# Performance work log

Measured on AMD Instinct MI355X. Metric: run time of the kernel, lower is better.

## Reference

```python
import jax, jax.numpy as jnp
import numpy as np
import math

N = 100000          # total nodes across all subgraphs
E = 1600000         # directed edges (avg degree 16)
H = 128             # hidden_channels
MAXZ = 1000         # max_z
G = 1000            # number of subgraphs (unique batch ids)
NPG = N // G        # nodes per subgraph
L = 3               # num_layers


def setup_inputs() -> dict:
    key = jax.random.key(0)
    ks = jax.random.split(key, 9)
    z = jax.random.randint(ks[0], (N,), 0, MAXZ, dtype=jnp.int32)
    edge_index = jax.random.randint(ks[1], (2, E), 0, N, dtype=jnp.int32)
    batch = jnp.repeat(jnp.arange(G, dtype=jnp.int32), NPG)  # sorted graph ids
    s = 1.0 / math.sqrt(H)
    z_emb_table = jax.random.normal(ks[2], (MAXZ, H), jnp.float32) * 0.1
    conv_w = jax.random.normal(ks[3], (L, H, H), jnp.float32) * s
    conv_b = jnp.zeros((L, H), jnp.float32)
    mlp_w1 = jax.random.normal(ks[4], (H, H), jnp.float32) * s
    mlp_b1 = jnp.zeros((H,), jnp.float32)
    mlp_w2 = jax.random.normal(ks[5], (H, 1), jnp.float32) * s
    mlp_b2 = jnp.zeros((1,), jnp.float32)
    return {"num_nodes": N, "z": z, "edge_index": edge_index, "batch": batch,
            "z_emb_table": z_emb_table, "conv_w": conv_w, "conv_b": conv_b,
            "mlp_w1": mlp_w1, "mlp_b1": mlp_b1, "mlp_w2": mlp_w2, "mlp_b2": mlp_b2}


def reference(num_nodes, z, edge_index, batch, z_emb_table, conv_w, conv_b,
              mlp_w1, mlp_b1, mlp_w2, mlp_b2):
    # --- GCN normalization (PyG GCNConv: add self-loops, sym deg norm) ---
    loops = jnp.arange(num_nodes, dtype=edge_index.dtype)
    src = jnp.concatenate([edge_index[0], loops])  # [E+N]
    dst = jnp.concatenate([edge_index[1], loops])
    deg = jax.ops.segment_sum(jnp.ones_like(dst, jnp.float32), dst,
                              num_segments=num_nodes)
    dinv = jnp.where(deg > 0, jax.lax.rsqrt(deg), 0.0)
    norm = (dinv[src] * dinv[dst])[:, None]        # [E+N, 1]

    # --- embedding lookup (eval mode: no dropedge/dropout) ---
    x = z_emb_table[z]                             # [N, H]

    # --- stacked GCNConv: linear -> gather -> normalize -> scatter-add ---
    for l in range(L):
        h = x @ conv_w[l]                          # [N, H]
        h = jax.ops.segment_sum(h[src] * norm, dst, num_segments=num_nodes)
        h = h + conv_b[l]
        x = jax.nn.relu(h) if l < L - 1 else h

    # --- center-node pooling: first occurrence of each batch id ---
    first = jnp.concatenate([jnp.array([True]), batch[1:] != batch[:-1]])
    ci = jnp.nonzero(first, size=G)[0]             # [G]
    xs = x[ci] * x[ci + 1]                         # src * dst node features

    # --- MLP head [H, H, 1] (batch_norm=False, eval: dropout off) ---
    h = jax.nn.relu(xs @ mlp_w1 + mlp_b1)
    return h @ mlp_w2 + mlp_b2                     # [G, 1]
```

## Files before the change

### kernel.cpp

```cpp
#include <hip/hip_runtime.h>
#include <hip/hip_fp16.h>

#define HD 128
#define BSH 9
#define NBLKA 256
#define CAP 96
#define EDSCAP 10240
#define CAPB 12288
#define XSW(row, c8) (((size_t)(row) << 7) + ((size_t)(((c8) ^ ((row) & 7))) << 3))

typedef _Float16 half8_t __attribute__((ext_vector_type(8)));
typedef float floatx4 __attribute__((ext_vector_type(4)));

__device__ inline unsigned pack_h2(float x, float y) {
  __half2 h = __floats2half2_rn(x, y);
  return __builtin_bit_cast(unsigned, h);
}
__device__ inline float2 up_h2(unsigned u) {
  __half2 h = __builtin_bit_cast(__half2, u);
  return __half22float2(h);
}

__device__ inline void add8(float* acc, uint4 r) {
  float2 f;
  f = up_h2(r.x); acc[0] += f.x; acc[1] += f.y;
  f = up_h2(r.y); acc[2] += f.x; acc[3] += f.y;
  f = up_h2(r.z); acc[4] += f.x; acc[5] += f.y;
  f = up_h2(r.w); acc[6] += f.x; acc[7] += f.y;
}

__global__ __launch_bounds__(256) void k_phase0(const int* __restrict__ src,
                                                const int* __restrict__ dst, int E, int nbuck,
                                                unsigned* __restrict__ bpool,
                                                int* __restrict__ counts,
                                                const float* __restrict__ conv_w,
                                                uint4* __restrict__ wfrag,
                                                const int* __restrict__ batch,
                                                int* __restrict__ ci,
                                                int* __restrict__ flag,
                                                int n) {
  __shared__ int cnt[512];
  int b = blockIdx.x;
  if (b < NBLKA) {
    for (int i = threadIdx.x; i < nbuck; i += 256) cnt[i] = 0;
    __syncthreads();
    int chunk = (E + NBLKA - 1) / NBLKA;
    int lo = b * chunk, hi = min(E, lo + chunk);
    for (int i = lo + threadIdx.x; i < hi; i += 256) {
      int s = src[i], d = dst[i];
      int bk = d >> BSH;
      int c = atomicAdd(&cnt[bk], 1);
      if (c < CAP)
        bpool[((size_t)bk * NBLKA + b) * CAP + c] =
            ((unsigned)(d & ((1 << BSH) - 1)) << 23) | (unsigned)s;
    }
    __syncthreads();
    for (int bk = threadIdx.x; bk < nbuck; bk += 256) counts[(size_t)bk * NBLKA + b] = cnt[bk];
  } else if (b < NBLKA + 24) {
    int t = (b - NBLKA) * 256 + threadIdx.x;
    int lane = t & 63;
    int s = (t >> 6) & 3;
    int c4 = (t >> 8) & 3;
    int chalf = (t >> 10) & 1;
    int layer = t >> 11;
    int col = chalf * 64 + c4 * 16 + (lane & 15);
    int k0 = s * 32 + (lane >> 4) * 8;
    const float* W = conv_w + (size_t)layer * HD * HD;
    unsigned u[4];
#pragma unroll
    for (int j = 0; j < 4; ++j)
      u[j] = pack_h2(W[(size_t)(k0 + 2 * j) * HD + col], W[(size_t)(k0 + 2 * j + 1) * HD + col]);
    uint4 o; o.x = u[0]; o.y = u[1]; o.z = u[2]; o.w = u[3];
    wfrag[t] = o;
  } else {
    int i = (b - NBLKA - 24) * 256 + threadIdx.x;
    if (i >= n) return;
    flag[i] = 0;
    if (i == 0) flag[n] = 0;
    if (i == 0 || batch[i] != batch[i - 1]) ci[batch[i]] = i;
  }
}

__global__ __launch_bounds__(256) void k_build(const unsigned* __restrict__ bpool,
                                               const int* __restrict__ counts,
                                               int n, float* __restrict__ dinv,
                                               int* __restrict__ rowstart,
                                               int* __restrict__ rowend,
                                               int* __restrict__ col) {
  __shared__ unsigned eds[EDSCAP];
  __shared__ int hist[1 << BSH];
  __shared__ int wsum[256];
  __shared__ int coff[NBLKA + 1];
  int b = blockIdx.x;
  int t = threadIdx.x;
  int v = (t < NBLKA) ? min(counts[(size_t)b * NBLKA + t], CAP) : 0;
  wsum[t] = v;
  __syncthreads();
  for (int off = 1; off < NBLKA; off <<= 1) {
    int x = (t >= off) ? wsum[t - off] : 0;
    __syncthreads();
    wsum[t] += x;
    __syncthreads();
  }
  if (t < NBLKA) coff[t] = wsum[t] - v;
  if (t == NBLKA - 1) coff[NBLKA] = wsum[NBLKA - 1];
  __syncthreads();
  int total = min(coff[NBLKA], EDSCAP);
  int w = t >> 6, lane = t & 63;
  for (int blk = w; blk < NBLKA; blk += 4) {
    int off0 = coff[blk], len = coff[blk + 1] - off0;
    const unsigned* seg = bpool + ((size_t)b * NBLKA + blk) * CAP;
    for (int i = lane; i < len; i += 64)
      if (off0 + i < EDSCAP) eds[off0 + i] = seg[i];
  }
  for (int i = t; i < (1 << BSH); i += 256) hist[i] = 0;
  __syncthreads();
  for (int i = t; i < total; i += 256) atomicAdd(&hist[eds[i] >> 23], 1);
  __syncthreads();
  int base = b << BSH;
  int nn = min(1 << BSH, n - base);
  int a0 = hist[2 * t], a1 = hist[2 * t + 1];
  int s = a0 + a1;
  wsum[t] = s;
  __syncthreads();
  for (int off = 1; off < 256; off <<= 1) {
    int x = (t >= off) ? wsum[t - off] : 0;
    __syncthreads();
    wsum[t] += x;
    __syncthreads();
  }
  int excl = wsum[t] - s;
  int cbase = b * CAPB;
  if (2 * t < nn) {
    rowstart[base + 2 * t] = cbase + excl;
    rowend[base + 2 * t] = cbase + excl + a0;
    dinv[base + 2 * t] = 1.0f / sqrtf((float)(a0 + 1));
  }
  if (2 * t + 1 < nn) {
    rowstart[base + 2 * t + 1] = cbase + excl + a0;
    rowend[base + 2 * t + 1] = cbase + excl + s;
    dinv[base + 2 * t + 1] = 1.0f / sqrtf((float)(a1 + 1));
  }
  hist[2 * t] = cbase + excl;
  hist[2 * t + 1] = cbase + excl + a0;
  __syncthreads();
  for (int i = t; i < total; i += 256) {
    unsigned pk = eds[i];
    int dl = pk >> 23;
    int pos = atomicAdd(&hist[dl], 1);
    col[pos] = (int)(pk & 0x7FFFFF);
  }
}

__global__ __launch_bounds__(64) void k_active(const int* __restrict__ ci,
                                               const int* __restrict__ rowstart,
                                               const int* __restrict__ rowend,
                                               const int* __restrict__ col,
                                               int g2, int* __restrict__ flag,
                                               int* __restrict__ list, int n) {
  int lane = threadIdx.x;
  int vid = blockIdx.x * 64 + lane;
  bool haveRow = vid < g2;
  int* nactive = flag + n;
  int node = 0, e = 0, end = 0;
  if (haveRow) {
    node = ci[vid >> 1] + (vid & 1);
    e = rowstart[node];
    end = rowend[node];
  }
  bool neu = haveRow && (atomicExch(&flag[node], 1) == 0);
  unsigned long long m = __ballot(neu);
  int base = 0;
  if (lane == 0 && m) base = atomicAdd(nactive, __popcll(m));
  base = __shfl(base, 0);
  if (neu) list[base + __popcll(m & ((1ULL << lane) - 1))] = node;
  for (;;) {
    bool act = haveRow && (e < end);
    if (!__any(act)) break;
    int s = act ? col[e] : 0;
    bool nw = act && (atomicExch(&flag[s], 1) == 0);
    unsigned long long mm = __ballot(nw);
    int b2 = 0;
    if (lane == 0 && mm) b2 = atomicAdd(nactive, __popcll(mm));
    b2 = __shfl(b2, 0);
    if (nw) list[b2 + __popcll(mm & ((1ULL << lane) - 1))] = s;
    ++e;
  }
}

__device__ inline void gemm16(const _Float16* xs, const uint4* __restrict__ wfragL,
                              const float* __restrict__ dinv, uint2* __restrict__ Yh,
                              int row0, int nvalid, const int* __restrict__ rowmap,
                              int tid) {
  int lane = tid & 63, w = tid >> 6;
  int chalf = w >> 1, h = lane >> 4;
  half8_t wf[8];
#pragma unroll
  for (int cc = 0; cc < 2; ++cc)
#pragma unroll
    for (int s = 0; s < 4; ++s) {
      int c4 = 2 * (w & 1) + cc;
      wf[cc * 4 + s] = __builtin_bit_cast(half8_t,
          wfragL[((chalf * 4 + c4) * 4 + s) * 64 + lane]);
    }
  half8_t bf[4];
#pragma unroll
  for (int s = 0; s < 4; ++s)
    bf[s] = *(const half8_t*)&xs[XSW(lane & 15, s * 4 + h)];
  floatx4 acc[2];
  acc[0] = (floatx4){0.f, 0.f, 0.f, 0.f};
  acc[1] = (floatx4){0.f, 0.f, 0.f, 0.f};
#pragma unroll
  for (int s = 0; s < 4; ++s) {
    acc[0] = __builtin_amdgcn_mfma_f32_16x16x32_f16(wf[s], bf[s], acc[0], 0, 0, 0);
    acc[1] = __builtin_amdgcn_mfma_f32_16x16x32_f16(wf[4 + s], bf[s], acc[1], 0, 0, 0);
  }
  int i = row0 + (lane & 15);
  if (i < nvalid) {
    int orow = rowmap ? rowmap[i] : i;
    float dv = dinv[orow];
#pragma unroll
    for (int cc = 0; cc < 2; ++cc) {
      int c4 = 2 * (w & 1) + cc;
      int colbase = chalf * 64 + c4 * 16 + h * 4;
      uint2 o;
      o.x = pack_h2(acc[cc][0] * dv, acc[cc][1] * dv);
      o.y = pack_h2(acc[cc][2] * dv, acc[cc][3] * dv);
      Yh[(size_t)orow * 32 + (colbase >> 2)] = o;
    }
  }
}

__global__ __launch_bounds__(256) void k_embgemm(const int* __restrict__ z,
                                                 const float4* __restrict__ emb,
                                                 const uint4* __restrict__ wfragL,
                                                 const float* __restrict__ dinv,
                                                 uint2* __restrict__ Yh, int n) {
  __shared__ __align__(16) _Float16 xs[16 * HD];
  int tid = threadIdx.x;
  int grp = tid >> 4, li = tid & 15;
  int node = blockIdx.x * 16 + grp;
  int nd = node < n ? node : n - 1;
  const float4* er = emb + (size_t)z[nd] * 32 + li * 2;
  float4 f0 = er[0], f1 = er[1];
  uint4 hx;
  hx.x = pack_h2(f0.x, f0.y); hx.y = pack_h2(f0.z, f0.w);
  hx.z = pack_h2(f1.x, f1.y); hx.w = pack_h2(f1.z, f1.w);
  *(uint4*)&xs[XSW(grp, li)] = hx;
  __syncthreads();
  gemm16(xs, wfragL, dinv, Yh, blockIdx.x * 16, n, nullptr, tid);
}

__global__ __launch_bounds__(256) void k_agg_gemm(const uint4* __restrict__ H,
                                                  const int* __restrict__ rowstart,
                                                  const int* __restrict__ rowend,
                                                  const int* __restrict__ col,
                                                  const float* __restrict__ dinv,
                                                  const float* __restrict__ bias,
                                                  const uint4* __restrict__ wfragL,
                                                  uint2* __restrict__ Yh, int n) {
  __shared__ __align__(16) _Float16 xs[16 * HD];
  int tid = threadIdx.x;
  int grp = tid >> 4, li = tid & 15;
  int node = blockIdx.x * 16 + grp;
  int nd = node < n ? node : n - 1;
  uint4 srow = H[(size_t)nd * 16 + li];
  float acc[8] = {0.f, 0.f, 0.f, 0.f, 0.f, 0.f, 0.f, 0.f};
  add8(acc, srow);
  int e = rowstart[nd], end = rowend[nd];
  for (; e + 3 < end; e += 4) {
    int c0 = col[e], c1 = col[e + 1], c2 = col[e + 2], c3 = col[e + 3];
    uint4 r0 = H[(size_t)c0 * 16 + li];
    uint4 r1 = H[(size_t)c1 * 16 + li];
    uint4 r2 = H[(size_t)c2 * 16 + li];
    uint4 r3 = H[(size_t)c3 * 16 + li];
    add8(acc, r0);
    add8(acc, r1);
    add8(acc, r2);
    add8(acc, r3);
  }
  for (; e < end; ++e) {
    uint4 r = H[(size_t)col[e] * 16 + li];
    add8(acc, r);
  }
  float dv = dinv[nd];
  float4 b0 = ((const float4*)bias)[2 * li];
  float4 b1 = ((const float4*)bias)[2 * li + 1];
  acc[0] = fmaxf(fmaf(dv, acc[0], b0.x), 0.f);
  acc[1] = fmaxf(fmaf(dv, acc[1], b0.y), 0.f);
  acc[2] = fmaxf(fmaf(dv, acc[2], b0.z), 0.f);
  acc[3] = fmaxf(fmaf(dv, acc[3], b0.w), 0.f);
  acc[4] = fmaxf(fmaf(dv, acc[4], b1.x), 0.f);
  acc[5] = fmaxf(fmaf(dv, acc[5], b1.y), 0.f);
  acc[6] = fmaxf(fmaf(dv, acc[6], b1.z), 0.f);
  acc[7] = fmaxf(fmaf(dv, acc[7], b1.w), 0.f);
  uint4 hx;
  hx.x = pack_h2(acc[0], acc[1]); hx.y = pack_h2(acc[2], acc[3]);
  hx.z = pack_h2(acc[4], acc[5]); hx.w = pack_h2(acc[6], acc[7]);
  *(uint4*)&xs[XSW(grp, li)] = hx;
  __syncthreads();
  gemm16(xs, wfragL, dinv, Yh, blockIdx.x * 16, n, nullptr, tid);
}

__global__ __launch_bounds__(256) void k_agg_gemmL(const uint4* __restrict__ H,
                                                   const int* __restrict__ rowstart,
                                                   const int* __restrict__ rowend,
                                                   const int* __restrict__ col,
                                                   const float* __restrict__ dinv,
                                                   const float* __restrict__ bias,
                                                   const uint4* __restrict__ wfragL,
                                                   uint2* __restrict__ Yh,
                                                   const int* __restrict__ list,
                                                   const int* __restrict__ nactive) {
  __shared__ __align__(16) _Float16 xs[16 * HD];
  int na = *nactive;
  int tid = threadIdx.x;
  int grp = tid >> 4, li = tid & 15;
  for (int tile = blockIdx.x; tile * 16 < na; tile += gridDim.x) {
    int i = tile * 16 + grp;
    int node = list[i < na ? i : na - 1];
    uint4 srow = H[(size_t)node * 16 + li];
    float acc[8] = {0.f, 0.f, 0.f, 0.f, 0.f, 0.f, 0.f, 0.f};
    add8(acc, srow);
    int e = rowstart[node], end = rowend[node];
    for (; e + 3 < end; e += 4) {
      int c0 = col[e], c1 = col[e + 1], c2 = col[e + 2], c3 = col[e + 3];
      uint4 r0 = H[(size_t)c0 * 16 + li];
      uint4 r1 = H[(size_t)c1 * 16 + li];
      uint4 r2 = H[(size_t)c2 * 16 + li];
      uint4 r3 = H[(size_t)c3 * 16 + li];
      add8(acc, r0);
      add8(acc, r1);
      add8(acc, r2);
      add8(acc, r3);
    }
    for (; e < end; ++e) {
      uint4 r = H[(size_t)col[e] * 16 + li];
      add8(acc, r);
    }
    float dv = dinv[node];
    float4 b0 = ((const float4*)bias)[2 * li];
    float4 b1 = ((const float4*)bias)[2 * li + 1];
    acc[0] = fmaxf(fmaf(dv, acc[0], b0.x), 0.f);
    acc[1] = fmaxf(fmaf(dv, acc[1], b0.y), 0.f);
    acc[2] = fmaxf(fmaf(dv, acc[2], b0.z), 0.f);
    acc[3] = fmaxf(fmaf(dv, acc[3], b0.w), 0.f);
    acc[4] = fmaxf(fmaf(dv, acc[4], b1.x), 0.f);
    acc[5] = fmaxf(fmaf(dv, acc[5], b1.y), 0.f);
    acc[6] = fmaxf(fmaf(dv, acc[6], b1.z), 0.f);
    acc[7] = fmaxf(fmaf(dv, acc[7], b1.w), 0.f);
    uint4 hx;
    hx.x = pack_h2(acc[0], acc[1]); hx.y = pack_h2(acc[2], acc[3]);
    hx.z = pack_h2(acc[4], acc[5]); hx.w = pack_h2(acc[6], acc[7]);
    *(uint4*)&xs[XSW(grp, li)] = hx;
    __syncthreads();
    gemm16(xs, wfragL, dinv, Yh, tile * 16, na, list, tid);
    __syncthreads();
  }
}

__global__ __launch_bounds__(128) void k_tail(const uint4* __restrict__ H,
                                              const int* __restrict__ rowstart,
                                              const int* __restrict__ rowend,
                                              const int* __restrict__ col,
                                              const float* __restrict__ dinv,
                                              const float* __restrict__ bias,
                                              const int* __restrict__ ci,
                                              const float* __restrict__ W1,
                                              const float* __restrict__ b1,
                                              const float* __restrict__ w2,
                                              const float* __restrict__ b2,
                                              float* __restrict__ out, int G) {
  __shared__ float part[8][HD];
  __shared__ float xs[HD];
  __shared__ float red[HD];
  int g = blockIdx.x;
  int t = threadIdx.x;
  int grp = t >> 4, li = t & 15;
  int nodeA = ci[g];
  int node = nodeA + (grp >> 2);
  int gi = grp & 3;
  float acc[8] = {0.f, 0.f, 0.f, 0.f, 0.f, 0.f, 0.f, 0.f};
  if (gi == 0) add8(acc, H[(size_t)node * 16 + li]);
  for (int e = rowstart[node] + gi; e < rowend[node]; e += 4) {
    uint4 r = H[(size_t)col[e] * 16 + li];
    add8(acc, r);
  }
#pragma unroll
  for (int j = 0; j < 8; ++j) part[grp][li * 8 + j] = acc[j];
  __syncthreads();
  float sumA = part[0][t] + part[1][t] + part[2][t] + part[3][t];
  float sumB = part[4][t] + part[5][t] + part[6][t] + part[7][t];
  float bb = bias[t];
  float va = fmaf(dinv[nodeA], sumA, bb);
  float vb = fmaf(dinv[nodeA + 1], sumB, bb);
  xs[t] = va * vb;
  __syncthreads();
  float hacc = b1[t];
#pragma unroll 8
  for (int k = 0; k < HD; ++k) hacc = fmaf(xs[k], W1[k * HD + t], hacc);
  hacc = fmaxf(hacc, 0.f);
  red[t] = hacc * w2[t];
  __syncthreads();
  for (int off = 64; off > 0; off >>= 1) {
    if (t < off) red[t] += red[t + off];
    __syncthreads();
  }
  if (t == 0) out[g] = red[0] + b2[0];
}

extern "C" void kernel_launch(void* const* d_in, const int* in_sizes, int n_in,
                              void* d_out, int out_size, void* d_ws, size_t ws_size,
                              hipStream_t stream) {
  (void)n_in; (void)ws_size;
  const int*   z      = (const int*)d_in[1];
  const int*   ei     = (const int*)d_in[2];
  const int*   batch  = (const int*)d_in[3];
  const float* emb    = (const float*)d_in[4];
  const float* conv_w = (const float*)d_in[5];
  const float* conv_b = (const float*)d_in[6];
  const float* w1     = (const float*)d_in[7];
  const float* b1     = (const float*)d_in[8];
  const float* w2     = (const float*)d_in[9];
  const float* b2     = (const float*)d_in[10];
  int n = in_sizes[1];
  int E = in_sizes[2] / 2;
  int G = out_size;
  const int* esrc = ei;
  const int* edst = ei + E;
  int nbuck = (n + (1 << BSH) - 1) >> BSH;

  char* p = (char*)d_ws;
  auto alloc = [&](size_t bytes) { void* r = (void*)p; p += (bytes + 255) / 256 * 256; return r; };
  unsigned* bufA     = (unsigned*)alloc((size_t)n * HD * 2);
  unsigned* bufB     = (unsigned*)alloc((size_t)n * HD * 2);
  float*    dinv     = (float*)alloc((size_t)n * 4);
  int*      rowstart = (int*)alloc((size_t)n * 4);
  int*      rowend   = (int*)alloc((size_t)n * 4);
  int*      col      = (int*)alloc((size_t)nbuck * CAPB * 4);
  uint4*    wfrag    = (uint4*)alloc((size_t)3 * 2048 * 16);
  int*      ci       = (int*)alloc((size_t)G * 4);
  int*      flag     = (int*)alloc((size_t)(n + 64) * 4);
  int*      list     = (int*)alloc((size_t)n * 4);
  unsigned* bpool    = (unsigned*)alloc((size_t)nbuck * NBLKA * CAP * 4);
  int*      counts   = (int*)alloc((size_t)nbuck * NBLKA * 4);

  int ciBlocks = (n + 255) / 256;
  int g2 = 2 * G;
  int* nactive = flag + n;

  k_phase0<<<NBLKA + 24 + ciBlocks, 256, 0, stream>>>(
      esrc, edst, E, nbuck, bpool, counts, conv_w, wfrag, batch, ci, flag, n);
  k_build<<<nbuck, 256, 0, stream>>>(bpool, counts, n, dinv, rowstart, rowend, col);
  k_embgemm<<<(n + 15) / 16, 256, 0, stream>>>(z, (const float4*)emb, wfrag, dinv,
                                               (uint2*)bufB, n);
  k_active<<<(g2 + 63) / 64, 64, 0, stream>>>(ci, rowstart, rowend, col, g2, flag, list, n);
  k_agg_gemm<<<(n + 15) / 16, 256, 0, stream>>>((const uint4*)bufB, rowstart, rowend, col,
                                                dinv, conv_b, wfrag + 2048, (uint2*)bufA, n);
  k_agg_gemmL<<<512, 256, 0, stream>>>((const uint4*)bufA, rowstart, rowend, col, dinv,
                                       conv_b + HD, wfrag + 4096, (uint2*)bufB, list, nactive);
  k_tail<<<G, 128, 0, stream>>>((const uint4*)bufB, rowstart, rowend, col, dinv,
                                conv_b + 2 * HD, ci, w1, b1, w2, b2, (float*)d_out, G);
}
```

Baseline: 226.8 us.

## Precompute embedding-times-weight table per z and gather it in first aggregation

Layer 0's linear transform is applied to the 1000-row embedding table instead of to every node, producing a small table T0 inside extra blocks of k_build. The first aggregation then gathers T0 rows indexed by z, with a packed (z, dinv) array per node, and scales each by the source dinv. This removes the per-node embedding GEMM kernel and the full-size fp16 intermediate write and read. It adds an extra indirection per edge, the D2 load, before the row gather.

New measurement: 200.1 us. -11.8%, faster.

```diff
diff --git a/kernel.cpp b/kernel.cpp
--- a/kernel.cpp
+++ b/kernel.cpp
@@ -27,6 +27,14 @@
   f = up_h2(r.y); acc[2] += f.x; acc[3] += f.y;
   f = up_h2(r.z); acc[4] += f.x; acc[5] += f.y;
   f = up_h2(r.w); acc[6] += f.x; acc[7] += f.y;
+}
+
+__device__ inline void fma8w(float* acc, uint4 r, float w) {
+  float2 f;
+  f = up_h2(r.x); acc[0] = fmaf(w, f.x, acc[0]); acc[1] = fmaf(w, f.y, acc[1]);
+  f = up_h2(r.y); acc[2] = fmaf(w, f.x, acc[2]); acc[3] = fmaf(w, f.y, acc[3]);
+  f = up_h2(r.z); acc[4] = fmaf(w, f.x, acc[4]); acc[5] = fmaf(w, f.y, acc[5]);
+  f = up_h2(r.w); acc[6] = fmaf(w, f.x, acc[6]); acc[7] = fmaf(w, f.y, acc[7]);
 }
 
 __global__ __launch_bounds__(256) void k_phase0(const int* __restrict__ src,
@@ -81,18 +89,83 @@
   }
 }
 
+__device__ inline void gemm16(const _Float16* xs, const uint4* __restrict__ wfragL,
+                              const float* __restrict__ dinv, uint2* __restrict__ Yh,
+                              int row0, int nvalid, const int* __restrict__ rowmap,
+                              int tid) {
+  int lane = tid & 63, w = tid >> 6;
+  int chalf = w >> 1, h = lane >> 4;
+  half8_t wf[8];
+#pragma unroll
+  for (int cc = 0; cc < 2; ++cc)
+#pragma unroll
+    for (int s = 0; s < 4; ++s) {
+      int c4 = 2 * (w & 1) + cc;
+      wf[cc * 4 + s] = __builtin_bit_cast(half8_t,
+          wfragL[((chalf * 4 + c4) * 4 + s) * 64 + lane]);
+    }
+  half8_t bf[4];
+#pragma unroll
+  for (int s = 0; s < 4; ++s)
+    bf[s] = *(const half8_t*)&xs[XSW(lane & 15, s * 4 + h)];
+  floatx4 acc[2];
+  acc[0] = (floatx4){0.f, 0.f, 0.f, 0.f};
+  acc[1] = (floatx4){0.f, 0.f, 0.f, 0.f};
+#pragma unroll
+  for (int s = 0; s < 4; ++s) {
+    acc[0] = __builtin_amdgcn_mfma_f32_16x16x32_f16(wf[s], bf[s], acc[0], 0, 0, 0);
+    acc[1] = __builtin_amdgcn_mfma_f32_16x16x32_f16(wf[4 + s], bf[s], acc[1], 0, 0, 0);
+  }
+  int i = row0 + (lane & 15);
+  if (i < nvalid) {
+    int orow = rowmap ? rowmap[i] : i;
+    float dv = dinv ? dinv[orow] : 1.0f;
+#pragma unroll
+    for (int cc = 0; cc < 2; ++cc) {
+      int c4 = 2 * (w & 1) + cc;
+      int colbase = chalf * 64 + c4 * 16 + h * 4;
+      uint2 o;
+      o.x = pack_h2(acc[cc][0] * dv, acc[cc][1] * dv);
+      o.y = pack_h2(acc[cc][2] * dv, acc[cc][3] * dv);
+      Yh[(size_t)orow * 32 + (colbase >> 2)] = o;
+    }
+  }
+}
+
 __global__ __launch_bounds__(256) void k_build(const unsigned* __restrict__ bpool,
                                                const int* __restrict__ counts,
-                                               int n, float* __restrict__ dinv,
+                                               int n, int nbuck, int maxz,
+                                               const int* __restrict__ z,
+                                               const float4* __restrict__ emb,
+                                               const uint4* __restrict__ wfrag0,
+                                               float* __restrict__ dinv,
+                                               uint2* __restrict__ d2,
+                                               uint2* __restrict__ t0,
                                                int* __restrict__ rowstart,
                                                int* __restrict__ rowend,
                                                int* __restrict__ col) {
-  __shared__ unsigned eds[EDSCAP];
+  __shared__ __align__(16) unsigned eds[EDSCAP];
   __shared__ int hist[1 << BSH];
   __shared__ int wsum[256];
   __shared__ int coff[NBLKA + 1];
   int b = blockIdx.x;
   int t = threadIdx.x;
+  if (b >= nbuck) {
+    int rb = b - nbuck;
+    _Float16* xs = (_Float16*)eds;
+    int grp = t >> 4, li = t & 15;
+    int row = rb * 16 + grp;
+    int r = row < maxz ? row : maxz - 1;
+    const float4* er = emb + (size_t)r * 32 + li * 2;
+    float4 f0 = er[0], f1 = er[1];
+    uint4 hx;
+    hx.x = pack_h2(f0.x, f0.y); hx.y = pack_h2(f0.z, f0.w);
+    hx.z = pack_h2(f1.x, f1.y); hx.w = pack_h2(f1.z, f1.w);
+    *(uint4*)&xs[XSW(grp, li)] = hx;
+    __syncthreads();
+    gemm16(xs, wfrag0, nullptr, t0, rb * 16, maxz, nullptr, t);
+    return;
+  }
   int v = (t < NBLKA) ? min(counts[(size_t)b * NBLKA + t], CAP) : 0;
   wsum[t] = v;
   __syncthreads();
@@ -132,14 +205,20 @@
   int excl = wsum[t] - s;
   int cbase = b * CAPB;
   if (2 * t < nn) {
-    rowstart[base + 2 * t] = cbase + excl;
-    rowend[base + 2 * t] = cbase + excl + a0;
-    dinv[base + 2 * t] = 1.0f / sqrtf((float)(a0 + 1));
+    int i = base + 2 * t;
+    float d = 1.0f / sqrtf((float)(a0 + 1));
+    rowstart[i] = cbase + excl;
+    rowend[i] = cbase + excl + a0;
+    dinv[i] = d;
+    d2[i] = make_uint2((unsigned)z[i] * 16, __float_as_uint(d));
   }
   if (2 * t + 1 < nn) {
-    rowstart[base + 2 * t + 1] = cbase + excl + a0;
-    rowend[base + 2 * t + 1] = cbase + excl + s;
-    dinv[base + 2 * t + 1] = 1.0f / sqrtf((float)(a1 + 1));
+    int i = base + 2 * t + 1;
+    float d = 1.0f / sqrtf((float)(a1 + 1));
+    rowstart[i] = cbase + excl + a0;
+    rowend[i] = cbase + excl + s;
+    dinv[i] = d;
+    d2[i] = make_uint2((unsigned)z[i] * 16, __float_as_uint(d));
   }
   hist[2 * t] = cbase + excl;
   hist[2 * t + 1] = cbase + excl + a0;
@@ -188,100 +267,39 @@
   }
 }
 
-__device__ inline void gemm16(const _Float16* xs, const uint4* __restrict__ wfragL,
-                              const float* __restrict__ dinv, uint2* __restrict__ Yh,
-                              int row0, int nvalid, const int* __restrict__ rowmap,
-                              int tid) {
-  int lane = tid & 63, w = tid >> 6;
-  int chalf = w >> 1, h = lane >> 4;
-  half8_t wf[8];
-#pragma unroll
-  for (int cc = 0; cc < 2; ++cc)
-#pragma unroll
-    for (int s = 0; s < 4; ++s) {
-      int c4 = 2 * (w & 1) + cc;
-      wf[cc * 4 + s] = __builtin_bit_cast(half8_t,
-          wfragL[((chalf * 4 + c4) * 4 + s) * 64 + lane]);
-    }
-  half8_t bf[4];
-#pragma unroll
-  for (int s = 0; s < 4; ++s)
-    bf[s] = *(const half8_t*)&xs[XSW(lane & 15, s * 4 + h)];
-  floatx4 acc[2];
-  acc[0] = (floatx4){0.f, 0.f, 0.f, 0.f};
-  acc[1] = (floatx4){0.f, 0.f, 0.f, 0.f};
-#pragma unroll
-  for (int s = 0; s < 4; ++s) {
-    acc[0] = __builtin_amdgcn_mfma_f32_16x16x32_f16(wf[s], bf[s], acc[0], 0, 0, 0);
-    acc[1] = __builtin_amdgcn_mfma_f32_16x16x32_f16(wf[4 + s], bf[s], acc[1], 0, 0, 0);
-  }
-  int i = row0 + (lane & 15);
-  if (i < nvalid) {
-    int orow = rowmap ? rowmap[i] : i;
-    float dv = dinv[orow];
-#pragma unroll
-    for (int cc = 0; cc < 2; ++cc) {
-      int c4 = 2 * (w & 1) + cc;
-      int colbase = chalf * 64 + c4 * 16 + h * 4;
-      uint2 o;
-      o.x = pack_h2(acc[cc][0] * dv, acc[cc][1] * dv);
-      o.y = pack_h2(acc[cc][2] * dv, acc[cc][3] * dv);
-      Yh[(size_t)orow * 32 + (colbase >> 2)] = o;
-    }
-  }
-}
-
-__global__ __launch_bounds__(256) void k_embgemm(const int* __restrict__ z,
-                                                 const float4* __restrict__ emb,
-                                                 const uint4* __restrict__ wfragL,
-                                                 const float* __restrict__ dinv,
-                                                 uint2* __restrict__ Yh, int n) {
+__global__ __launch_bounds__(256) void k_agg0_gemm(const uint4* __restrict__ T0,
+                                                   const uint2* __restrict__ D2,
+                                                   const int* __restrict__ rowstart,
+                                                   const int* __restrict__ rowend,
+                                                   const int* __restrict__ col,
+                                                   const float* __restrict__ dinv,
+                                                   const float* __restrict__ bias,
+                                                   const uint4* __restrict__ wfragL,
+                                                   uint2* __restrict__ Yh, int n) {
   __shared__ __align__(16) _Float16 xs[16 * HD];
   int tid = threadIdx.x;
   int grp = tid >> 4, li = tid & 15;
   int node = blockIdx.x * 16 + grp;
   int nd = node < n ? node : n - 1;
-  const float4* er = emb + (size_t)z[nd] * 32 + li * 2;
-  float4 f0 = er[0], f1 = er[1];
-  uint4 hx;
-  hx.x = pack_h2(f0.x, f0.y); hx.y = pack_h2(f0.z, f0.w);
-  hx.z = pack_h2(f1.x, f1.y); hx.w = pack_h2(f1.z, f1.w);
-  *(uint4*)&xs[XSW(grp, li)] = hx;
-  __syncthreads();
-  gemm16(xs, wfragL, dinv, Yh, blockIdx.x * 16, n, nullptr, tid);
-}
-
-__global__ __launch_bounds__(256) void k_agg_gemm(const uint4* __restrict__ H,
-                                                  const int* __restrict__ rowstart,
-                                                  const int* __restrict__ rowend,
-                                                  const int* __restrict__ col,
-                                                  const float* __restrict__ dinv,
-                                                  const float* __restrict__ bias,
-                                                  const uint4* __restrict__ wfragL,
-                                                  uint2* __restrict__ Yh, int n) {
-  __shared__ __align__(16) _Float16 xs[16 * HD];
-  int tid = threadIdx.x;
-  int grp = tid >> 4, li = tid & 15;
-  int node = blockIdx.x * 16 + grp;
-  int nd = node < n ? node : n - 1;
-  uint4 srow = H[(size_t)nd * 16 + li];
   float acc[8] = {0.f, 0.f, 0.f, 0.f, 0.f, 0.f, 0.f, 0.f};
-  add8(acc, srow);
+  uint2 ds = D2[nd];
+  fma8w(acc, T0[ds.x + li], __uint_as_float(ds.y));
   int e = rowstart[nd], end = rowend[nd];
   for (; e + 3 < end; e += 4) {
     int c0 = col[e], c1 = col[e + 1], c2 = col[e + 2], c3 = col[e + 3];
-    uint4 r0 = H[(size_t)c0 * 16 + li];
-    uint4 r1 = H[(size_t)c1 * 16 + li];
-    uint4 r2 = H[(size_t)c2 * 16 + li];
-    uint4 r3 = H[(size_t)c3 * 16 + li];
-    add8(acc, r0);
-    add8(acc, r1);
-    add8(acc, r2);
-    add8(acc, r3);
+    uint2 p0 = D2[c0], p1 = D2[c1], p2 = D2[c2], p3 = D2[c3];
+    uint4 r0 = T0[p0.x + li];
+    uint4 r1 = T0[p1.x + li];
+    uint4 r2 = T0[p2.x + li];
+    uint4 r3 = T0[p3.x + li];
+    fma8w(acc, r0, __uint_as_float(p0.y));
+    fma8w(acc, r1, __uint_as_float(p1.y));
+    fma8w(acc, r2, __uint_as_float(p2.y));
+    fma8w(acc, r3, __uint_as_float(p3.y));
   }
   for (; e < end; ++e) {
-    uint4 r = H[(size_t)col[e] * 16 + li];
-    add8(acc, r);
+    uint2 p = D2[col[e]];
+    fma8w(acc, T0[p.x + li], __uint_as_float(p.y));
   }
   float dv = dinv[nd];
   float4 b0 = ((const float4*)bias)[2 * li];
@@ -426,15 +444,19 @@
   int n = in_sizes[1];
   int E = in_sizes[2] / 2;
   int G = out_size;
+  int maxz = in_sizes[4] / HD;
   const int* esrc = ei;
   const int* edst = ei + E;
   int nbuck = (n + (1 << BSH) - 1) >> BSH;
+  int t0Blocks = (maxz + 15) / 16;
 
   char* p = (char*)d_ws;
   auto alloc = [&](size_t bytes) { void* r = (void*)p; p += (bytes + 255) / 256 * 256; return r; };
   unsigned* bufA     = (unsigned*)alloc((size_t)n * HD * 2);
   unsigned* bufB     = (unsigned*)alloc((size_t)n * HD * 2);
   float*    dinv     = (float*)alloc((size_t)n * 4);
+  uint2*    d2       = (uint2*)alloc((size_t)n * 8);
+  uint2*    t0       = (uint2*)alloc((size_t)(t0Blocks * 16) * 32 * 8);
   int*      rowstart = (int*)alloc((size_t)n * 4);
   int*      rowend   = (int*)alloc((size_t)n * 4);
   int*      col      = (int*)alloc((size_t)nbuck * CAPB * 4);
@@ -451,12 +473,12 @@
 
   k_phase0<<<NBLKA + 24 + ciBlocks, 256, 0, stream>>>(
       esrc, edst, E, nbuck, bpool, counts, conv_w, wfrag, batch, ci, flag, n);
-  k_build<<<nbuck, 256, 0, stream>>>(bpool, counts, n, dinv, rowstart, rowend, col);
-  k_embgemm<<<(n + 15) / 16, 256, 0, stream>>>(z, (const float4*)emb, wfrag, dinv,
-                                               (uint2*)bufB, n);
+  k_build<<<nbuck + t0Blocks, 256, 0, stream>>>(bpool, counts, n, nbuck, maxz, z,
+                                                (const float4*)emb, wfrag, dinv, d2, t0,
+                                                rowstart, rowend, col);
   k_active<<<(g2 + 63) / 64, 64, 0, stream>>>(ci, rowstart, rowend, col, g2, flag, list, n);
-  k_agg_gemm<<<(n + 15) / 16, 256, 0, stream>>>((const uint4*)bufB, rowstart, rowend, col,
-                                                dinv, conv_b, wfrag + 2048, (uint2*)bufA, n);
+  k_agg0_gemm<<<(n + 15) / 16, 256, 0, stream>>>((const uint4*)t0, d2, rowstart, rowend, col,
+                                                 dinv, conv_b, wfrag + 2048, (uint2*)bufA, n);
   k_agg_gemmL<<<512, 256, 0, stream>>>((const uint4*)bufA, rowstart, rowend, col, dinv,
                                        conv_b + HD, wfrag + 4096, (uint2*)bufB, list, nactive);
   k_tail<<<G, 128, 0, stream>>>((const uint4*)bufB, rowstart, rowend, col, dinv,
```
